# Optimization experiments

Measured on AMD Instinct MI355X. Metric: run time of the kernel, lower is better.

The kernel has to match this reference:

```python
import jax, jax.numpy as jnp
import numpy as np

B, S, D = 1, 2048, 1024
H, HD = 16, 64          # attention heads, head dim
DFF = 4096              # ffn hidden
IH, ID = 4, 64          # indexer heads / dim ('baseline' strategy)
TOP_K = 64
ROPE_BASE = 10000.0
LN_EPS = 1e-5


def setup_inputs() -> dict:
    key = jax.random.key(0)
    ks = jax.random.split(key, 12)
    g = lambda k, shape: (jax.random.normal(k, shape, dtype=jnp.float32) * 0.02)
    return {
        "x": jax.random.normal(ks[0], (B, S, D), dtype=jnp.float32),
        "w_qkv": g(ks[1], (D, 3 * D)),
        "w_o": g(ks[2], (D, D)),
        "ffn_w1": g(ks[3], (D, DFF)),
        "ffn_b1": jnp.zeros((DFF,), jnp.float32),
        "ffn_w2": g(ks[4], (DFF, D)),
        "ffn_b2": jnp.zeros((D,), jnp.float32),
        "ln1_g": jnp.ones((D,), jnp.float32),
        "ln1_b": jnp.zeros((D,), jnp.float32),
        "ln2_g": jnp.ones((D,), jnp.float32),
        "ln2_b": jnp.zeros((D,), jnp.float32),
        "idx_wq": g(ks[5], (D, IH * ID)),
        "idx_wk": g(ks[6], (D, ID)),
        "idx_ww": g(ks[7], (D, IH)),
    }


def _layernorm(x, g, b):
    m = jnp.mean(x, axis=-1, keepdims=True)
    v = jnp.var(x, axis=-1, keepdims=True)
    return (x - m) * jax.lax.rsqrt(v + LN_EPS) * g + b


def _rope(x):  # x: [B,S,H,HD], torchtune interleaved-pair convention
    half = HD // 2
    theta = 1.0 / (ROPE_BASE ** (jnp.arange(0, HD, 2, dtype=jnp.float32) / HD))  # [half]
    ang = jnp.arange(S, dtype=jnp.float32)[:, None] * theta                      # [S,half]
    cos = jnp.cos(ang)[None, :, None, :]
    sin = jnp.sin(ang)[None, :, None, :]
    xp = x.reshape(*x.shape[:-1], half, 2)
    x0, x1 = xp[..., 0], xp[..., 1]
    out = jnp.stack([x0 * cos - x1 * sin, x1 * cos + x0 * sin], axis=-1)
    return out.reshape(x.shape)


def reference(x, w_qkv, w_o, ffn_w1, ffn_b1, ffn_w2, ffn_b2,
              ln1_g, ln1_b, ln2_g, ln2_b, idx_wq, idx_wk, idx_ww):
    norm_x = _layernorm(x, ln1_g, ln1_b)

    qkv = norm_x @ w_qkv                              # [B,S,3D]
    q, k, v = jnp.split(qkv, 3, axis=-1)
    q = _rope(q.reshape(B, S, H, HD))
    k = _rope(k.reshape(B, S, H, HD))
    v = v.reshape(B, S, H, HD)

    # Lightning-style indexer: I[t,s] = sum_h w[t,h] * relu(q_i[t,h] . k_i[s])
    qi = (norm_x @ idx_wq).reshape(B, S, IH, ID)      # [B,S,IH,ID]
    ki = norm_x @ idx_wk                              # [B,S,ID]
    wi = norm_x @ idx_ww                              # [B,S,IH]
    qk = jnp.einsum("bthd,bsd->bths", qi, ki)         # [B,S,IH,S]
    index_scores = jnp.einsum("bth,bths->bts", wi, jax.nn.relu(qk))  # [B,S,S]

    # causal top-k token selection -> boolean mask
    causal = jnp.tril(jnp.ones((S, S), dtype=bool))
    masked_scores = jnp.where(causal, index_scores, -jnp.inf)
    _, topk_idx = jax.lax.top_k(masked_scores, TOP_K)  # [B,S,K]
    b_ix = jnp.arange(B)[:, None, None]
    q_ix = jnp.arange(S)[None, :, None]
    mask = jnp.zeros((B, S, S), dtype=bool).at[b_ix, q_ix, topk_idx].set(True)
    mask = mask & causal                               # [B,S,S]

    # masked SDPA
    logits = jnp.einsum("bqhd,bkhd->bhqk", q, k) / np.sqrt(HD)
    logits = jnp.where(mask[:, None, :, :], logits, -jnp.inf)
    attn = jax.nn.softmax(logits, axis=-1)
    attn_out = jnp.einsum("bhqk,bkhd->bqhd", attn, v).reshape(B, S, D)
    x = x + attn_out @ w_o

    h = _layernorm(x, ln2_g, ln2_b)
    ffn = jax.nn.gelu(h @ ffn_w1 + ffn_b1, approximate=False) @ ffn_w2 + ffn_b2
    return x + ffn
```

## Files before the change

### kernel.cpp

```cpp
#include <hip/hip_runtime.h>
#include <math.h>

#define S_LEN 2048
#define D_MODEL 1024
#define NHEAD 16
#define HDIM 64
#define DFF 4096
#define IH 4
#define IDM 64
#define TOPK 64
#define NIDX 336

typedef float f32x4 __attribute__((ext_vector_type(4)));
typedef short bf16x8 __attribute__((ext_vector_type(8)));

__device__ __forceinline__ unsigned short f2bf(float f) {
    unsigned u = __builtin_bit_cast(unsigned, f);
    u += 0x7fff + ((u >> 16) & 1);
    return (unsigned short)(u >> 16);
}
__device__ __forceinline__ float bf2f(unsigned short us) {
    return __builtin_bit_cast(float, (unsigned)us << 16);
}

__device__ __forceinline__ float gelu_exact(float v) {
    return 0.5f * v * (1.f + erff(v * 0.70710678118654752f));
}

__device__ __forceinline__ void gl_lds16(const void* g, void* l) {
    __builtin_amdgcn_global_load_lds(
        (const __attribute__((address_space(1))) void*)g,
        (__attribute__((address_space(3))) void*)l, 16, 0, 0);
}

__global__ __launch_bounds__(256) void ln_kernel(const float* __restrict__ x,
    const float* __restrict__ g, const float* __restrict__ b,
    float* __restrict__ outf, unsigned short* __restrict__ outb)
{
    int row = blockIdx.x, tid = threadIdx.x;
    const float4 v = *(const float4*)(x + (size_t)row * D_MODEL + tid * 4);
    float s = v.x + v.y + v.z + v.w;
    float ss = v.x * v.x + v.y * v.y + v.z * v.z + v.w * v.w;
    int lane = tid & 63, wv = tid >> 6;
    for (int o = 32; o; o >>= 1) { s += __shfl_xor(s, o); ss += __shfl_xor(ss, o); }
    __shared__ float rs[4], rss[4];
    if (lane == 0) { rs[wv] = s; rss[wv] = ss; }
    __syncthreads();
    float S = rs[0] + rs[1] + rs[2] + rs[3];
    float SS = rss[0] + rss[1] + rss[2] + rss[3];
    float mean = S * (1.f / D_MODEL);
    float var = SS * (1.f / D_MODEL) - mean * mean;
    float r = rsqrtf(var + 1e-5f);
    float4 gv = *(const float4*)(g + tid * 4);
    float4 bv = *(const float4*)(b + tid * 4);
    float4 o4;
    o4.x = (v.x - mean) * r * gv.x + bv.x;
    o4.y = (v.y - mean) * r * gv.y + bv.y;
    o4.z = (v.z - mean) * r * gv.z + bv.z;
    o4.w = (v.w - mean) * r * gv.w + bv.w;
    if (outf) *(float4*)(outf + (size_t)row * D_MODEL + tid * 4) = o4;
    if (outb) {
        ushort4 u4 = { f2bf(o4.x), f2bf(o4.y), f2bf(o4.z), f2bf(o4.w) };
        *(ushort4*)(outb + (size_t)row * D_MODEL + tid * 4) = u4;
    }
}

__global__ __launch_bounds__(256) void wtrans_kernel(const float* __restrict__ in,
    unsigned short* __restrict__ out, int K, int N)
{
    __shared__ float t[32][33];
    int k0 = blockIdx.y * 32, n0 = blockIdx.x * 32;
    int tid = threadIdx.x;
    int r = tid >> 5, c = tid & 31;
#pragma unroll
    for (int p = 0; p < 4; ++p)
        t[r + p * 8][c] = in[(size_t)(k0 + r + p * 8) * N + n0 + c];
    __syncthreads();
#pragma unroll
    for (int p = 0; p < 4; ++p)
        out[(size_t)(n0 + r + p * 8) * K + k0 + c] = f2bf(t[c][r + p * 8]);
}

__global__ __launch_bounds__(256) void wpack_kernel(const float* __restrict__ wq,
    const float* __restrict__ wk, const float* __restrict__ ww, float* __restrict__ Wc)
{
    int idx = blockIdx.x * 256 + threadIdx.x;
    if (idx >= D_MODEL * NIDX) return;
    int r = idx / NIDX, c = idx % NIDX;
    float v = 0.f;
    if (c < 256) v = wq[r * 256 + c];
    else if (c < 320) v = wk[r * 64 + (c - 256)];
    else if (c < 324) v = ww[r * 4 + (c - 320)];
    Wc[idx] = v;
}

__global__ __launch_bounds__(256) void gemm_bf16_n64(
    const unsigned short* __restrict__ A, const unsigned short* __restrict__ Bt,
    float* __restrict__ C, unsigned short* __restrict__ Cb,
    const float* __restrict__ bias, const float* __restrict__ R,
    int M, int N, int K, int act,
    float* __restrict__ P, int kchunk)
{
    __shared__ __attribute__((aligned(16))) unsigned short As[2][128 * 32];
    __shared__ __attribute__((aligned(16))) unsigned short Bs[2][64 * 32];
    int tid = threadIdx.x;
    int bm = blockIdx.y * 128, bn = blockIdx.x * 64;
    int wid = tid >> 6, lane = tid & 63;
    int wm = wid * 32;
    const unsigned short* Ab = A + (size_t)bm * K;
    const unsigned short* Bb = Bt + (size_t)bn * K;
    f32x4 acc[2][4];
#pragma unroll
    for (int i = 0; i < 2; ++i)
#pragma unroll
        for (int j = 0; j < 4; ++j)
            acc[i][j] = (f32x4){0.f, 0.f, 0.f, 0.f};

    int kbeg = blockIdx.z * kchunk;
    int kend = kbeg + kchunk;
    int fr = lane & 15;
    int srow = tid >> 2;
    int cels = (((tid & 3) ^ (srow & 3)) << 3);
    int dste = tid * 8;
    int selm = (((lane >> 4) ^ (fr & 3)) << 3);

    gl_lds16(Ab + (size_t)srow * K + kbeg + cels, &As[0][dste]);
    gl_lds16(Ab + (size_t)(srow + 64) * K + kbeg + cels, &As[0][dste + 2048]);
    gl_lds16(Bb + (size_t)srow * K + kbeg + cels, &Bs[0][dste]);
    __syncthreads();

    int cur = 0;
    for (int k0 = kbeg; k0 < kend; k0 += 32) {
        int nxt = k0 + 32;
        if (nxt < kend) {
            gl_lds16(Ab + (size_t)srow * K + nxt + cels, &As[cur ^ 1][dste]);
            gl_lds16(Ab + (size_t)(srow + 64) * K + nxt + cels, &As[cur ^ 1][dste + 2048]);
            gl_lds16(Bb + (size_t)srow * K + nxt + cels, &Bs[cur ^ 1][dste]);
        }
        bf16x8 af[2], bfv[4];
#pragma unroll
        for (int mi = 0; mi < 2; ++mi)
            af[mi] = *(const bf16x8*)&As[cur][(wm + mi * 16 + fr) * 32 + selm];
#pragma unroll
        for (int ni = 0; ni < 4; ++ni)
            bfv[ni] = *(const bf16x8*)&Bs[cur][(ni * 16 + fr) * 32 + selm];
#pragma unroll
        for (int mi = 0; mi < 2; ++mi)
#pragma unroll
            for (int ni = 0; ni < 4; ++ni)
                acc[mi][ni] = __builtin_amdgcn_mfma_f32_16x16x32_bf16(
                    af[mi], bfv[ni], acc[mi][ni], 0, 0, 0);
        __syncthreads();
        cur ^= 1;
    }
    int cl = lane & 15, rh = (lane >> 4) * 4;
    if (P) {
        float* Pz = P + (size_t)blockIdx.z * M * N;
#pragma unroll
        for (int mi = 0; mi < 2; ++mi)
#pragma unroll
            for (int ni = 0; ni < 4; ++ni) {
                int col = bn + ni * 16 + cl;
#pragma unroll
                for (int r = 0; r < 4; ++r) {
                    int row = bm + wm + mi * 16 + rh + r;
                    Pz[(size_t)row * N + col] = acc[mi][ni][r];
                }
            }
        return;
    }
#pragma unroll
    for (int mi = 0; mi < 2; ++mi) {
#pragma unroll
        for (int ni = 0; ni < 4; ++ni) {
            int col = bn + ni * 16 + cl;
            float bv = bias ? bias[col] : 0.f;
#pragma unroll
            for (int r = 0; r < 4; ++r) {
                int row = bm + wm + mi * 16 + rh + r;
                float v = acc[mi][ni][r] + bv;
                if (act) v = gelu_exact(v);
                size_t off = (size_t)row * N + col;
                if (R) v += R[off];
                if (C) C[off] = v;
                if (Cb) Cb[off] = f2bf(v);
            }
        }
    }
}

__global__ __launch_bounds__(256) void kreduce_kernel(const float* __restrict__ P,
    int nslice, float* __restrict__ C, const float* __restrict__ bias,
    const float* __restrict__ R, int M, int N)
{
    size_t total4 = (size_t)M * N / 4;
    size_t stride = (size_t)gridDim.x * 256;
    for (size_t i4 = blockIdx.x * 256 + threadIdx.x; i4 < total4; i4 += stride) {
        size_t off = i4 * 4;
        float4 v = *(const float4*)(P + off);
        for (int z = 1; z < nslice; ++z) {
            float4 p = *(const float4*)(P + (size_t)z * M * N + off);
            v.x += p.x; v.y += p.y; v.z += p.z; v.w += p.w;
        }
        if (bias) {
            float4 b4 = *(const float4*)(bias + (off % N));
            v.x += b4.x; v.y += b4.y; v.z += b4.z; v.w += b4.w;
        }
        if (R) {
            float4 r4 = *(const float4*)(R + off);
            v.x += r4.x; v.y += r4.y; v.z += r4.z; v.w += r4.w;
        }
        *(float4*)(C + off) = v;
    }
}

__global__ __launch_bounds__(256) void gemm64(const float* __restrict__ A,
    const float* __restrict__ B, float* __restrict__ C,
    int M, int N, int K,
    float* __restrict__ P, int kchunk)
{
    __shared__ float As[16][68];
    __shared__ float Bs[16][68];
    int tid = threadIdx.x;
    int bm = blockIdx.y, bn = blockIdx.x;
    int tx = tid & 15, ty = tid >> 4;
    int arow = tid >> 2;
    int acol = (tid & 3) << 2;
    int brow = tid >> 4;
    int bcol = (tid & 15) << 2;
    const float* Abase = A + (size_t)(bm * 64 + arow) * K + acol;
    float c[4][4] = {};
    int kbeg = blockIdx.z * kchunk;
    int kend = kbeg + kchunk;
    for (int k0 = kbeg; k0 < kend; k0 += 16) {
        float4 av = *(const float4*)(Abase + k0);
        As[acol + 0][arow] = av.x;
        As[acol + 1][arow] = av.y;
        As[acol + 2][arow] = av.z;
        As[acol + 3][arow] = av.w;
        int gcol = bn * 64 + bcol;
        const float* Bb = B + (size_t)(k0 + brow) * N;
        float4 bv;
        if (gcol + 3 < N) {
            bv = *(const float4*)(Bb + gcol);
        } else {
            bv.x = (gcol + 0 < N) ? Bb[gcol + 0] : 0.f;
            bv.y = (gcol + 1 < N) ? Bb[gcol + 1] : 0.f;
            bv.z = (gcol + 2 < N) ? Bb[gcol + 2] : 0.f;
            bv.w = (gcol + 3 < N) ? Bb[gcol + 3] : 0.f;
        }
        *(float4*)&Bs[brow][bcol] = bv;
        __syncthreads();
#pragma unroll
        for (int kk = 0; kk < 16; ++kk) {
            float4 a4 = *(const float4*)&As[kk][ty * 4];
            float4 b4 = *(const float4*)&Bs[kk][tx * 4];
            float av4[4] = { a4.x, a4.y, a4.z, a4.w };
            float bv4[4] = { b4.x, b4.y, b4.z, b4.w };
#pragma unroll
            for (int i = 0; i < 4; ++i)
#pragma unroll
                for (int j = 0; j < 4; ++j)
                    c[i][j] += av4[i] * bv4[j];
        }
        __syncthreads();
    }
    float* Out = P ? (P + (size_t)blockIdx.z * M * N) : C;
#pragma unroll
    for (int i = 0; i < 4; ++i) {
        int row = bm * 64 + ty * 4 + i;
#pragma unroll
        for (int j = 0; j < 4; ++j) {
            int col = bn * 64 + tx * 4 + j;
            if (col < N)
                Out[(size_t)row * N + col] = c[i][j];
        }
    }
}

__global__ __launch_bounds__(256) void rope_table_kernel(float* __restrict__ ct, float* __restrict__ st)
{
    int g = blockIdx.x * 256 + threadIdx.x;
    int t = g >> 5, i = g & 31;
    float theta = powf(10000.f, -(float)i / 32.f);
    float ang = (float)t * theta;
    ct[g] = cosf(ang);
    st[g] = sinf(ang);
}

__global__ __launch_bounds__(512) void rope_pack_kernel(
    const unsigned short* __restrict__ qkvb,
    const float* __restrict__ ct, const float* __restrict__ st,
    unsigned short* __restrict__ Qb, unsigned short* __restrict__ Kb,
    unsigned short* __restrict__ Vb)
{
    int t = blockIdx.x, tid = threadIdx.x;
    int h = tid >> 5, i = tid & 31;
    float c = ct[t * 32 + i], s = st[t * 32 + i];
    const unsigned short* base = qkvb + (size_t)t * (3 * D_MODEL);
    ushort2 q2 = *(const ushort2*)(base + h * HDIM + 2 * i);
    float q0 = bf2f(q2.x), q1 = bf2f(q2.y);
    ushort2 qo = { f2bf(q0 * c - q1 * s), f2bf(q1 * c + q0 * s) };
    *(ushort2*)(Qb + (size_t)t * D_MODEL + h * HDIM + 2 * i) = qo;
    ushort2 k2 = *(const ushort2*)(base + D_MODEL + h * HDIM + 2 * i);
    float k0 = bf2f(k2.x), k1 = bf2f(k2.y);
    ushort2 ko = { f2bf(k0 * c - k1 * s), f2bf(k1 * c + k0 * s) };
    *(ushort2*)(Kb + ((size_t)h * S_LEN + t) * HDIM + 2 * i) = ko;
    ushort2 v2 = *(const ushort2*)(base + 2 * D_MODEL + 2 * tid);
    int vh = tid >> 5, vd = (2 * tid) & 63;
    *(ushort2*)(Vb + ((size_t)vh * S_LEN + t) * HDIM + vd) = v2;
}

__global__ __launch_bounds__(256) void scores_kernel(const float* __restrict__ QIW,
    float* __restrict__ scores)
{
    int t0 = blockIdx.y * 64, s0 = blockIdx.x * 64;
    if (s0 > t0 + 63) return;
    __shared__ float qit[64][68];
    __shared__ float kit[64][68];
    __shared__ float wis[64][4];
    int tid = threadIdx.x;
    int tx = tid & 15, ty = tid >> 4;
    int lr = tid & 63;
    int cseg = tid >> 6;
    if (tid < 64) {
        float4 w4 = *(const float4*)(QIW + (size_t)(t0 + tid) * NIDX + 320);
        wis[tid][0] = w4.x; wis[tid][1] = w4.y; wis[tid][2] = w4.z; wis[tid][3] = w4.w;
    }
    float acc[4][4] = {};
#pragma unroll
    for (int h = 0; h < 4; ++h) {
        __syncthreads();
        const float* qrow = QIW + (size_t)(t0 + lr) * NIDX + h * 64 + cseg * 16;
        const float* krow = QIW + (size_t)(s0 + lr) * NIDX + 256 + cseg * 16;
#pragma unroll
        for (int q4 = 0; q4 < 4; ++q4) {
            int d = cseg * 16 + q4 * 4;
            float4 v = *(const float4*)(qrow + q4 * 4);
            qit[d + 0][lr] = v.x; qit[d + 1][lr] = v.y;
            qit[d + 2][lr] = v.z; qit[d + 3][lr] = v.w;
            if (h == 0) {
                float4 u = *(const float4*)(krow + q4 * 4);
                kit[d + 0][lr] = u.x; kit[d + 1][lr] = u.y;
                kit[d + 2][lr] = u.z; kit[d + 3][lr] = u.w;
            }
        }
        __syncthreads();
        float dot[4][4] = {};
#pragma unroll 8
        for (int d = 0; d < 64; ++d) {
            float4 a4 = *(const float4*)&qit[d][ty * 4];
            float4 b4 = *(const float4*)&kit[d][tx * 4];
            float av[4] = { a4.x, a4.y, a4.z, a4.w };
            float bv[4] = { b4.x, b4.y, b4.z, b4.w };
#pragma unroll
            for (int i = 0; i < 4; ++i)
#pragma unroll
                for (int j = 0; j < 4; ++j)
                    dot[i][j] += av[i] * bv[j];
        }
#pragma unroll
        for (int i = 0; i < 4; ++i) {
            float w = wis[ty * 4 + i][h];
#pragma unroll
            for (int j = 0; j < 4; ++j)
                acc[i][j] += w * fmaxf(dot[i][j], 0.f);
        }
    }
#pragma unroll
    for (int i = 0; i < 4; ++i) {
        float4 o4 = { acc[i][0], acc[i][1], acc[i][2], acc[i][3] };
        *(float4*)&scores[(size_t)(t0 + ty * 4 + i) * S_LEN + s0 + tx * 4] = o4;
    }
}

__global__ __launch_bounds__(256) void topk_kernel(const float* __restrict__ scores,
    int* __restrict__ topidx, int* __restrict__ topcnt)
{
    int t = blockIdx.x, tid = threadIdx.x;
    int n = t + 1;
    if (n <= TOPK) {
        if (tid < n) topidx[t * TOPK + tid] = tid;
        if (tid == 0) topcnt[t] = n;
        return;
    }
    __shared__ unsigned sc[S_LEN];
    __shared__ unsigned hist[256];
    __shared__ int selbin_s;
    __shared__ int cnt_out;
    __shared__ unsigned wsum[4];
    for (int j = tid; j < n; j += 256) {
        unsigned u = __builtin_bit_cast(unsigned, scores[(size_t)t * S_LEN + j]);
        sc[j] = (u & 0x80000000u) ? ~u : (u | 0x80000000u);
    }
    if (tid == 0) cnt_out = 0;
    int lane = tid & 63, wv = tid >> 6;
    unsigned prefix = 0;
    int kk = TOPK;
#pragma unroll
    for (int round = 0; round < 4; ++round) {
        int shift_pref = 32 - 8 * round;
        int shift_bin = 24 - 8 * round;
        hist[tid] = 0;
        __syncthreads();
        for (int j = tid; j < n; j += 256) {
            unsigned v = sc[j];
            if ((((unsigned long long)(v ^ prefix)) >> shift_pref) == 0)
                atomicAdd(&hist[(v >> shift_bin) & 0xff], 1u);
        }
        __syncthreads();
        if (wv == 0) {
            unsigned h0 = hist[4 * lane], h1 = hist[4 * lane + 1];
            unsigned h2 = hist[4 * lane + 2], h3 = hist[4 * lane + 3];
            unsigned s3 = h3, s2 = h2 + s3, s1 = h1 + s2, s0 = h0 + s1;
            unsigned acc = s0;
            for (int off = 1; off < 64; off <<= 1) {
                unsigned o = __shfl_down(acc, off);
                if (lane + off < 64) acc += o;
            }
            unsigned above = acc - s0;
            hist[4 * lane]     = s0 + above;
            hist[4 * lane + 1] = s1 + above;
            hist[4 * lane + 2] = s2 + above;
            hist[4 * lane + 3] = s3 + above;
        }
        __syncthreads();
        {
            unsigned sufb = hist[tid];
            unsigned sufn = (tid < 255) ? hist[tid + 1] : 0u;
            if (sufb >= (unsigned)kk && sufn < (unsigned)kk)
                selbin_s = tid;
        }
        __syncthreads();
        int b = selbin_s;
        unsigned above = (b < 255) ? hist[b + 1] : 0u;
        kk -= (int)above;
        prefix |= ((unsigned)b) << shift_bin;
        __syncthreads();
    }
    unsigned T = prefix;
    int chunk = (n + 255) >> 8;
    int jb = tid * chunk;
    int je = jb + chunk; if (je > n) je = n;
    int ties = 0;
    for (int j = jb; j < je; ++j) {
        unsigned v = sc[j];
        if (v > T) { int o = atomicAdd(&cnt_out, 1); topidx[t * TOPK + o] = j; }
        else if (v == T) ++ties;
    }
    unsigned inc = (unsigned)ties;
    for (int off = 1; off < 64; off <<= 1) {
        unsigned o = __shfl_up(inc, off);
        if (lane >= off) inc += o;
    }
    if (lane == 63) wsum[wv] = inc;
    __syncthreads();
    unsigned woff = 0;
    for (int w = 0; w < wv; ++w) woff += wsum[w];
    int rank = (int)(woff + inc) - ties;
    for (int j = jb; j < je && rank < kk; ++j) {
        if (sc[j] == T) {
            int o = atomicAdd(&cnt_out, 1);
            topidx[t * TOPK + o] = j;
            ++rank;
        }
    }
    if (tid == 0) topcnt[t] = TOPK;
}

__global__ __launch_bounds__(256) void attn_kernel(
    const unsigned short* __restrict__ Qb, const unsigned short* __restrict__ Kb,
    const unsigned short* __restrict__ Vb,
    const int* __restrict__ topidx, const int* __restrict__ topcnt,
    unsigned short* __restrict__ out)
{
    int t = blockIdx.x, tid = threadIdx.x;
    __shared__ int sel[TOPK];
    if (tid < TOPK) sel[tid] = topidx[t * TOPK + tid];
    __syncthreads();
    int cnt = topcnt[t];
    int lane = tid & 63, wv = tid >> 6;
    int h = blockIdx.y * 4 + wv;
    int klo = lane >> 3, oct = lane & 7;
    int rows[8];
    bool valid[8];
#pragma unroll
    for (int kg = 0; kg < 8; ++kg) {
        int k = kg * 8 + klo;
        valid[kg] = (k < cnt);
        rows[kg] = sel[valid[kg] ? k : 0];
    }
    bf16x8 q8 = *(const bf16x8*)(Qb + (size_t)t * D_MODEL + h * HDIM + oct * 8);
    float qf[8];
#pragma unroll
    for (int e = 0; e < 8; ++e) qf[e] = bf2f((unsigned short)q8[e]);

    const unsigned short* kbase = Kb + (size_t)h * S_LEN * HDIM + oct * 8;
    float p[8];
#pragma unroll
    for (int kg = 0; kg < 8; ++kg) {
        bf16x8 k8 = *(const bf16x8*)(kbase + (size_t)rows[kg] * HDIM);
        float d = 0.f;
#pragma unroll
        for (int e = 0; e < 8; ++e)
            d += bf2f((unsigned short)k8[e]) * qf[e];
        d += __shfl_xor(d, 1);
        d += __shfl_xor(d, 2);
        d += __shfl_xor(d, 4);
        p[kg] = valid[kg] ? d * 0.125f : -INFINITY;
    }
    float m = p[0];
#pragma unroll
    for (int kg = 1; kg < 8; ++kg) m = fmaxf(m, p[kg]);
    m = fmaxf(m, __shfl_xor(m, 8));
    m = fmaxf(m, __shfl_xor(m, 16));
    m = fmaxf(m, __shfl_xor(m, 32));
    float sum = 0.f;
#pragma unroll
    for (int kg = 0; kg < 8; ++kg) { p[kg] = __expf(p[kg] - m); sum += p[kg]; }
    sum += __shfl_xor(sum, 8);
    sum += __shfl_xor(sum, 16);
    sum += __shfl_xor(sum, 32);
    float rs = 1.f / sum;
    const unsigned short* vbase = Vb + (size_t)h * S_LEN * HDIM + oct * 8;
    float facc[8] = {};
#pragma unroll
    for (int kg = 0; kg < 8; ++kg) {
        bf16x8 v8 = *(const bf16x8*)(vbase + (size_t)rows[kg] * HDIM);
        float pw = p[kg] * rs;
#pragma unroll
        for (int e = 0; e < 8; ++e)
            facc[e] += pw * bf2f((unsigned short)v8[e]);
    }
#pragma unroll
    for (int e = 0; e < 8; ++e) {
        facc[e] += __shfl_xor(facc[e], 8);
        facc[e] += __shfl_xor(facc[e], 16);
        facc[e] += __shfl_xor(facc[e], 32);
    }
    if (klo == 0) {
        ushort4 o0 = { f2bf(facc[0]), f2bf(facc[1]), f2bf(facc[2]), f2bf(facc[3]) };
        ushort4 o1 = { f2bf(facc[4]), f2bf(facc[5]), f2bf(facc[6]), f2bf(facc[7]) };
        *(ushort4*)(out + (size_t)t * D_MODEL + h * HDIM + oct * 8) = o0;
        *(ushort4*)(out + (size_t)t * D_MODEL + h * HDIM + oct * 8 + 4) = o1;
    }
}

extern "C" void kernel_launch(void* const* d_in, const int* in_sizes, int n_in,
                              void* d_out, int out_size, void* d_ws, size_t ws_size,
                              hipStream_t stream)
{
    const float* x      = (const float*)d_in[0];
    const float* w_qkv  = (const float*)d_in[1];
    const float* w_o    = (const float*)d_in[2];
    const float* ffn_w1 = (const float*)d_in[3];
    const float* ffn_b1 = (const float*)d_in[4];
    const float* ffn_w2 = (const float*)d_in[5];
    const float* ffn_b2 = (const float*)d_in[6];
    const float* ln1_g  = (const float*)d_in[7];
    const float* ln1_b  = (const float*)d_in[8];
    const float* ln2_g  = (const float*)d_in[9];
    const float* ln2_b  = (const float*)d_in[10];
    const float* idx_wq = (const float*)d_in[11];
    const float* idx_wk = (const float*)d_in[12];
    const float* idx_ww = (const float*)d_in[13];
    float* outp = (float*)d_out;

    const size_t MB = 1ull << 20;
    char* ws = (char*)d_ws;
    float*          normx    = (float*)(ws + 0);
    unsigned short* attno_bf = (unsigned short*)(ws + 0);
    float*          Pf2      = (float*)(ws + 0);
    unsigned short* normx_bf = (unsigned short*)(ws + 8 * MB);
    unsigned short* h2_bf    = normx_bf;
    unsigned short* qkv_bf   = (unsigned short*)(ws + 12 * MB);
    int*            topidx   = (int*)(ws + 12 * MB);
    int*            topcnt   = (int*)(ws + 12 * MB + 512 * 1024);
    unsigned short* wqkv_t   = (unsigned short*)(ws + 24 * MB);
    unsigned short* wo_t     = (unsigned short*)(ws + 30 * MB);
    unsigned short* w1_t     = (unsigned short*)(ws + 32 * MB);
    unsigned short* w2_t     = (unsigned short*)(ws + 40 * MB);
    unsigned short* Qb       = (unsigned short*)(ws + 48 * MB);
    unsigned short* Kb       = (unsigned short*)(ws + 52 * MB);
    unsigned short* Vb       = (unsigned short*)(ws + 56 * MB);
    float*          ctab     = (float*)(ws + 60 * MB);
    float*          stab     = (float*)(ws + 60 * MB + 256 * 1024);
    float*          P_idx    = (float*)(ws + 60 * MB);
    float*          scoresb  = (float*)(ws + 60 * MB);
    float*          Pwo      = (float*)(ws + 60 * MB);
    unsigned short* ffn1_bf  = (unsigned short*)(ws + 60 * MB);
    float*          QIW      = (float*)(ws + 76 * MB);
    float*          Wc       = (float*)(ws + 79 * MB);

    dim3 blk256(256);
    auto g64n = [](int N, int M) { return dim3(N / 64, M / 128); };

    ln_kernel<<<S_LEN, blk256, 0, stream>>>(x, ln1_g, ln1_b, normx, normx_bf);
    rope_table_kernel<<<(S_LEN * 32) / 256, blk256, 0, stream>>>(ctab, stab);
    wtrans_kernel<<<dim3(3 * D_MODEL / 32, D_MODEL / 32), blk256, 0, stream>>>(w_qkv, wqkv_t, D_MODEL, 3 * D_MODEL);
    wtrans_kernel<<<dim3(D_MODEL / 32, D_MODEL / 32), blk256, 0, stream>>>(w_o, wo_t, D_MODEL, D_MODEL);
    wtrans_kernel<<<dim3(DFF / 32, D_MODEL / 32), blk256, 0, stream>>>(ffn_w1, w1_t, D_MODEL, DFF);
    wtrans_kernel<<<dim3(D_MODEL / 32, DFF / 32), blk256, 0, stream>>>(ffn_w2, w2_t, DFF, D_MODEL);
    wpack_kernel<<<(D_MODEL * NIDX + 255) / 256, blk256, 0, stream>>>(idx_wq, idx_wk, idx_ww, Wc);
    gemm_bf16_n64<<<g64n(3 * D_MODEL, S_LEN), blk256, 0, stream>>>(normx_bf, wqkv_t,
        nullptr, qkv_bf, nullptr, nullptr, S_LEN, 3 * D_MODEL, D_MODEL, 0, nullptr, D_MODEL);
    rope_pack_kernel<<<S_LEN, dim3(512), 0, stream>>>(qkv_bf, ctab, stab, Qb, Kb, Vb);
    gemm64<<<dim3((NIDX + 63) / 64, S_LEN / 64, 4), blk256, 0, stream>>>(normx, Wc,
        nullptr, S_LEN, NIDX, D_MODEL, P_idx, D_MODEL / 4);
    kreduce_kernel<<<1024, blk256, 0, stream>>>(P_idx, 4, QIW, nullptr, nullptr, S_LEN, NIDX);
    scores_kernel<<<dim3(32, 32), blk256, 0, stream>>>(QIW, scoresb);
    topk_kernel<<<S_LEN, blk256, 0, stream>>>(scoresb, topidx, topcnt);
    attn_kernel<<<dim3(S_LEN, 4), blk256, 0, stream>>>(Qb, Kb, Vb, topidx, topcnt, attno_bf);
    gemm_bf16_n64<<<dim3(D_MODEL / 64, S_LEN / 128, 2), blk256, 0, stream>>>(attno_bf, wo_t,
        nullptr, nullptr, nullptr, nullptr, S_LEN, D_MODEL, D_MODEL, 0, Pwo, D_MODEL / 2);
    kreduce_kernel<<<1024, blk256, 0, stream>>>(Pwo, 2, outp, nullptr, x, S_LEN, D_MODEL);
    ln_kernel<<<S_LEN, blk256, 0, stream>>>(outp, ln2_g, ln2_b, nullptr, h2_bf);
    gemm_bf16_n64<<<g64n(DFF, S_LEN), blk256, 0, stream>>>(h2_bf, w1_t,
        nullptr, ffn1_bf, ffn_b1, nullptr, S_LEN, DFF, D_MODEL, 1, nullptr, D_MODEL);
    gemm_bf16_n64<<<dim3(D_MODEL / 64, S_LEN / 128, 4), blk256, 0, stream>>>(ffn1_bf, w2_t,
        nullptr, nullptr, nullptr, nullptr, S_LEN, D_MODEL, DFF, 0, Pf2, DFF / 4);
    kreduce_kernel<<<1024, blk256, 0, stream>>>(Pf2, 4, outp, ffn_b2, outp, S_LEN, D_MODEL);
}
```

Measured before the change: 272.2 us.

## Triple-buffer GEMM LDS stages with explicit vmcnt waits and drop XOR swizzle

The bf16 GEMM main loop moves from a double-buffered LDS pipeline with a full __syncthreads per K step to a three-stage ring. Two tiles stay in flight, and each step waits with s_waitcnt vmcnt(3) plus a raw s_barrier. The idea is to hide global-to-LDS load latency better and make the barrier cheaper. The XOR swizzle on LDS columns is also removed, which may bring back LDS bank conflicts on fragment reads. The larger shared-memory footprint can also lower occupancy.

```diff
diff --git a/kernel.cpp b/kernel.cpp
--- a/kernel.cpp
+++ b/kernel.cpp
@@ -101,8 +101,8 @@
     int M, int N, int K, int act,
     float* __restrict__ P, int kchunk)
 {
-    __shared__ __attribute__((aligned(16))) unsigned short As[2][128 * 32];
-    __shared__ __attribute__((aligned(16))) unsigned short Bs[2][64 * 32];
+    __shared__ __attribute__((aligned(16))) unsigned short As[3][128 * 32];
+    __shared__ __attribute__((aligned(16))) unsigned short Bs[3][64 * 32];
     int tid = threadIdx.x;
     int bm = blockIdx.y * 128, bn = blockIdx.x * 64;
     int wid = tid >> 6, lane = tid & 63;
@@ -117,42 +117,50 @@
             acc[i][j] = (f32x4){0.f, 0.f, 0.f, 0.f};
 
     int kbeg = blockIdx.z * kchunk;
-    int kend = kbeg + kchunk;
-    int fr = lane & 15;
-    int srow = tid >> 2;
-    int cels = (((tid & 3) ^ (srow & 3)) << 3);
-    int dste = tid * 8;
-    int selm = (((lane >> 4) ^ (fr & 3)) << 3);
-
-    gl_lds16(Ab + (size_t)srow * K + kbeg + cels, &As[0][dste]);
-    gl_lds16(Ab + (size_t)(srow + 64) * K + kbeg + cels, &As[0][dste + 2048]);
-    gl_lds16(Bb + (size_t)srow * K + kbeg + cels, &Bs[0][dste]);
-    __syncthreads();
-
-    int cur = 0;
-    for (int k0 = kbeg; k0 < kend; k0 += 32) {
-        int nxt = k0 + 32;
-        if (nxt < kend) {
-            gl_lds16(Ab + (size_t)srow * K + nxt + cels, &As[cur ^ 1][dste]);
-            gl_lds16(Ab + (size_t)(srow + 64) * K + nxt + cels, &As[cur ^ 1][dste + 2048]);
-            gl_lds16(Bb + (size_t)srow * K + nxt + cels, &Bs[cur ^ 1][dste]);
-        }
+    int NT = kchunk >> 5;
+    int fr = lane & 15, fk = (lane >> 4) * 8;
+    int e0 = tid * 8;
+    int r0 = e0 >> 5, c0 = e0 & 31;
+
+    auto STAGE = [&](int kt, int buf) {
+        int k0 = kbeg + kt * 32;
+        gl_lds16(Ab + (size_t)r0 * K + k0 + c0, &As[buf][e0]);
+        gl_lds16(Ab + (size_t)(r0 + 64) * K + k0 + c0, &As[buf][e0 + 2048]);
+        gl_lds16(Bb + (size_t)r0 * K + k0 + c0, &Bs[buf][e0]);
+    };
+    auto COMPUTE = [&](int buf) {
         bf16x8 af[2], bfv[4];
 #pragma unroll
         for (int mi = 0; mi < 2; ++mi)
-            af[mi] = *(const bf16x8*)&As[cur][(wm + mi * 16 + fr) * 32 + selm];
+            af[mi] = *(const bf16x8*)&As[buf][(wm + mi * 16 + fr) * 32 + fk];
 #pragma unroll
         for (int ni = 0; ni < 4; ++ni)
-            bfv[ni] = *(const bf16x8*)&Bs[cur][(ni * 16 + fr) * 32 + selm];
+            bfv[ni] = *(const bf16x8*)&Bs[buf][(ni * 16 + fr) * 32 + fk];
 #pragma unroll
         for (int mi = 0; mi < 2; ++mi)
 #pragma unroll
             for (int ni = 0; ni < 4; ++ni)
                 acc[mi][ni] = __builtin_amdgcn_mfma_f32_16x16x32_bf16(
                     af[mi], bfv[ni], acc[mi][ni], 0, 0, 0);
-        __syncthreads();
-        cur ^= 1;
-    }
+    };
+
+    STAGE(0, 0);
+    STAGE(1, 1);
+    asm volatile("s_waitcnt vmcnt(3)" ::: "memory");
+    __builtin_amdgcn_s_barrier();
+
+    int kt = 0;
+    for (; kt < NT - 2; ++kt) {
+        STAGE(kt + 2, (kt + 2) % 3);
+        COMPUTE(kt % 3);
+        asm volatile("s_waitcnt vmcnt(3)" ::: "memory");
+        __builtin_amdgcn_s_barrier();
+    }
+    COMPUTE((NT - 2) % 3);
+    asm volatile("s_waitcnt vmcnt(0)" ::: "memory");
+    __builtin_amdgcn_s_barrier();
+    COMPUTE((NT - 1) % 3);
+
     int cl = lane & 15, rh = (lane >> 4) * 4;
     if (P) {
         float* Pz = P + (size_t)blockIdx.z * M * N;
```

New measurement: 273.9 us. About the same (+0.6%).
